# Kernel optimization log

Measured on AMD Instinct MI355X. Metric: run time of the kernel, lower is better.

Reference implementation:

```python
import jax, jax.numpy as jnp
import numpy as np

N_NODES = 50000


def gcn_layer(x, src, dst, ew, W, b, n_nodes):
    # PyG GCNConv: add self-loops (weight 1), symmetric deg^-1/2 normalization,
    # linear transform, scatter-add aggregation at destination, then bias.
    loop = jnp.arange(n_nodes, dtype=src.dtype)
    s = jnp.concatenate([src, loop])
    d = jnp.concatenate([dst, loop])
    w = jnp.concatenate([ew, jnp.ones((n_nodes,), dtype=ew.dtype)])
    deg = jax.ops.segment_sum(w, d, num_segments=n_nodes)  # [N]
    dinv = jnp.where(deg > 0, jax.lax.rsqrt(jnp.where(deg > 0, deg, 1.0)), 0.0)
    norm = dinv[s] * w * dinv[d]  # [E+N]
    h = x @ W  # [N, out]
    msg = h[s] * norm[:, None]  # gather + scale, [E+N, out]
    out = jax.ops.segment_sum(msg, d, num_segments=n_nodes)  # scatter-add
    return out + b


def setup_inputs() -> dict:
    key = jax.random.key(0)
    k1, k2, k3, k4, k5, k6, k7 = jax.random.split(key, 7)
    N, E, C_IN, C_OUT = N_NODES, 600000, 128, 128
    x = jax.random.normal(k1, (N, C_IN), dtype=jnp.float32)
    edge_index = jax.random.randint(k2, (2, E), 0, N, dtype=jnp.int64)
    edge_weight = jax.random.uniform(k3, (E,), dtype=jnp.float32)
    # Glorot-style init like PyG's Linear default
    s1 = 1.0 / np.sqrt(C_IN)
    s2 = 1.0 / np.sqrt(C_OUT)
    W1 = jax.random.uniform(k4, (C_IN, C_OUT), jnp.float32, -s1, s1)
    b1 = jnp.zeros((C_OUT,), dtype=jnp.float32)
    W2 = jax.random.uniform(k5, (C_OUT, C_OUT), jnp.float32, -s2, s2)
    b2 = jnp.zeros((C_OUT,), dtype=jnp.float32)
    return {"x": x, "edge_index": edge_index, "edge_weight": edge_weight,
            "W1": W1, "b1": b1, "W2": W2, "b2": b2}


def reference(x, edge_index, edge_weight, W1, b1, W2, b2):
    src, dst = edge_index[0], edge_index[1]
    h = jax.nn.relu(gcn_layer(x, src, dst, edge_weight, W1, b1, N_NODES))
    return jax.nn.relu(gcn_layer(h, src, dst, edge_weight, W2, b2, N_NODES))
```

## Files before the change

kernel.cpp:

```cpp
#include <hip/hip_runtime.h>
#include <math.h>

#define CH   128
#define CH4  32
#define TPB  256
#define SCANB 1024
#define WIMG 16384
#define NREP 4

typedef __attribute__((ext_vector_type(8))) short short8;
typedef __attribute__((ext_vector_type(4))) float floatx4;

static __device__ __forceinline__ unsigned short f2bf(float f) {
    unsigned u = __float_as_uint(f);
    return (unsigned short)((u + 0x7fffu + ((u >> 16) & 1u)) >> 16);
}
static __device__ __forceinline__ float bf2f(unsigned short s) {
    return __uint_as_float(((unsigned)s) << 16);
}
static __device__ __forceinline__ float4 bf4_to_f4(ushort4 u) {
    return make_float4(bf2f(u.x), bf2f(u.y), bf2f(u.z), bf2f(u.w));
}

__global__ void k_prep(const float* __restrict__ W1, const float* __restrict__ W2,
                       short* __restrict__ Wsplit) {
    int i = blockIdx.x * blockDim.x + threadIdx.x;
    if (i >= 2 * CH * CH) return;
    int layer = i >> 14;
    int idx   = i & 16383;
    int k = idx >> 7, c = idx & 127;
    float w = (layer ? W2 : W1)[k * CH + c];
    unsigned short hi = f2bf(w);
    unsigned short lo = f2bf(w - bf2f(hi));
    int colh = c >> 6, nn = c & 63;
    int kt = k >> 5, q = (k & 31) >> 3, j = k & 7;
    int ns = nn >> 4, ln = q * 16 + (nn & 15);
    size_t base = (size_t)(layer * 2 + colh) * WIMG;
    size_t off  = ((size_t)(kt * 4 + ns) * 64 + ln) * 8 + j;
    Wsplit[base + off]        = (short)hi;
    Wsplit[base + 8192 + off] = (short)lo;
}

#define STAGE_W(sW, Wfrag, tid)                                    \
    {                                                              \
        const float4* gsrc = (const float4*)(Wfrag);               \
        float4* ldst = (float4*)(sW);                              \
        _Pragma("unroll")                                          \
        for (int i = 0; i < 8; ++i)                                \
            ldst[i * TPB + (tid)] = gsrc[i * TPB + (tid)];         \
    }

static __device__ __forceinline__ void gemm_body_f32(
        const float* __restrict__ X, const short* __restrict__ Wfrag,
        unsigned short* __restrict__ H, int n, int tile, int colh, int tid) {
    __shared__ __align__(16) short sW[2][4][4][64][8];
    STAGE_W(sW, Wfrag, tid);
    __syncthreads();

    const int lane = tid & 63;
    const int wv   = tid >> 6;
    const int q    = lane >> 4;
    const int m    = lane & 15;
    const int row0 = tile * 64 + wv * 16;
    if (row0 >= n) return;

    int rrow = row0 + m;
    if (rrow > n - 1) rrow = n - 1;

    const float4* xr = (const float4*)(X + (size_t)rrow * CH);
    float4 xa[4][2];
    #pragma unroll
    for (int kt = 0; kt < 4; ++kt) {
        xa[kt][0] = xr[kt * 8 + q * 2 + 0];
        xa[kt][1] = xr[kt * 8 + q * 2 + 1];
    }

    floatx4 acc[4];
    #pragma unroll
    for (int ns = 0; ns < 4; ++ns) acc[ns] = (floatx4){0.f, 0.f, 0.f, 0.f};

    #pragma unroll
    for (int kt = 0; kt < 4; ++kt) {
        float xf[8] = { xa[kt][0].x, xa[kt][0].y, xa[kt][0].z, xa[kt][0].w,
                        xa[kt][1].x, xa[kt][1].y, xa[kt][1].z, xa[kt][1].w };
        short8 ah, al;
        #pragma unroll
        for (int j = 0; j < 8; ++j) {
            float v = xf[j];
            unsigned short h = f2bf(v);
            ah[j] = (short)h;
            al[j] = (short)f2bf(v - bf2f(h));
        }
        #pragma unroll
        for (int ns = 0; ns < 4; ++ns) {
            short8 bh = *(const short8*)&sW[0][kt][ns][lane][0];
            short8 bl = *(const short8*)&sW[1][kt][ns][lane][0];
            acc[ns] = __builtin_amdgcn_mfma_f32_16x16x32_bf16(ah, bh, acc[ns], 0, 0, 0);
            acc[ns] = __builtin_amdgcn_mfma_f32_16x16x32_bf16(al, bh, acc[ns], 0, 0, 0);
            acc[ns] = __builtin_amdgcn_mfma_f32_16x16x32_bf16(ah, bl, acc[ns], 0, 0, 0);
        }
    }

    #pragma unroll
    for (int ns = 0; ns < 4; ++ns) {
        #pragma unroll
        for (int reg = 0; reg < 4; ++reg) {
            int r = row0 + q * 4 + reg;
            if (r < n)
                H[(size_t)r * CH + colh * 64 + ns * 16 + m] = f2bf(acc[ns][reg]);
        }
    }
}

static __device__ __forceinline__ void gemm_body_bf(
        const unsigned short* __restrict__ X, const short* __restrict__ Wfrag,
        unsigned short* __restrict__ H, int n, int tile, int colh, int tid) {
    __shared__ __align__(16) short sW[2][4][4][64][8];
    STAGE_W(sW, Wfrag, tid);
    __syncthreads();

    const int lane = tid & 63;
    const int wv   = tid >> 6;
    const int q    = lane >> 4;
    const int m    = lane & 15;
    const int row0 = tile * 64 + wv * 16;
    if (row0 >= n) return;

    int rrow = row0 + m;
    if (rrow > n - 1) rrow = n - 1;

    const short8* xr8 = (const short8*)(X + (size_t)rrow * CH);
    short8 a[4];
    #pragma unroll
    for (int kt = 0; kt < 4; ++kt) a[kt] = xr8[kt * 4 + q];

    floatx4 acc[4];
    #pragma unroll
    for (int ns = 0; ns < 4; ++ns) acc[ns] = (floatx4){0.f, 0.f, 0.f, 0.f};

    #pragma unroll
    for (int kt = 0; kt < 4; ++kt) {
        #pragma unroll
        for (int ns = 0; ns < 4; ++ns) {
            short8 bh = *(const short8*)&sW[0][kt][ns][lane][0];
            short8 bl = *(const short8*)&sW[1][kt][ns][lane][0];
            acc[ns] = __builtin_amdgcn_mfma_f32_16x16x32_bf16(a[kt], bh, acc[ns], 0, 0, 0);
            acc[ns] = __builtin_amdgcn_mfma_f32_16x16x32_bf16(a[kt], bl, acc[ns], 0, 0, 0);
        }
    }

    #pragma unroll
    for (int ns = 0; ns < 4; ++ns) {
        #pragma unroll
        for (int reg = 0; reg < 4; ++reg) {
            int r = row0 + q * 4 + reg;
            if (r < n)
                H[(size_t)r * CH + colh * 64 + ns * 16 + m] = f2bf(acc[ns][reg]);
        }
    }
}

__global__ __launch_bounds__(TPB, 4)
void k_gemm_rank(const float* __restrict__ X, const short* __restrict__ Wsplit,
                 unsigned short* __restrict__ H, int n,
                 const int* __restrict__ dst, const float* __restrict__ ew,
                 int* __restrict__ counts_rep, float* __restrict__ deg_rep,
                 int* __restrict__ rank, int E, int nbE, int Np) {
    int bx = blockIdx.x;
    if (bx < nbE) {
        int e = bx * TPB + threadIdx.x;
        if (e < E) {
            int d = dst[e];
            if ((unsigned)d < (unsigned)n) {
                int rep = e & (NREP - 1);
                rank[e] = atomicAdd(&counts_rep[rep * Np + d], 1);
                unsafeAtomicAdd(&deg_rep[rep * Np + d], ew[e]);
            }
        }
    } else {
        bx -= nbE;
        int colh = bx & 1;
        gemm_body_f32(X, Wsplit + (size_t)colh * WIMG, H, n, bx >> 1, colh,
                      threadIdx.x);
    }
}

__global__ __launch_bounds__(TPB, 4)
void k_gemm_bf(const unsigned short* __restrict__ X, const short* __restrict__ Wsplit,
               unsigned short* __restrict__ H, int n) {
    int colh = (int)blockIdx.x & 1;
    gemm_body_bf(X, Wsplit + (size_t)colh * WIMG, H, n,
                 (int)blockIdx.x >> 1, colh, threadIdx.x);
}

__global__ __launch_bounds__(SCANB)
void k_scan1(const int* __restrict__ counts_rep, const float* __restrict__ deg_rep,
             int Np, int* __restrict__ counts_tot, int4* __restrict__ repoff,
             int* __restrict__ row_start, float* __restrict__ dinv,
             int* __restrict__ partials, int* __restrict__ pp_s,
             int* __restrict__ done, int nb, int n) {
    __shared__ int s[SCANB];
    __shared__ int slast;
    int gid = blockIdx.x * SCANB + threadIdx.x;
    int c0 = 0, c1 = 0, c2 = 0, c3 = 0;
    if (gid < n) {
        c0 = counts_rep[gid];
        c1 = counts_rep[Np + gid];
        c2 = counts_rep[2 * Np + gid];
        c3 = counts_rep[3 * Np + gid];
        float dsum = 1.0f + deg_rep[gid] + deg_rep[Np + gid]
                   + deg_rep[2 * Np + gid] + deg_rep[3 * Np + gid];
        dinv[gid] = rsqrtf(dsum);
    }
    int v = c0 + c1 + c2 + c3;
    s[threadIdx.x] = v;
    __syncthreads();
    for (int off = 1; off < SCANB; off <<= 1) {
        int t = (threadIdx.x >= off) ? s[threadIdx.x - off] : 0;
        __syncthreads();
        s[threadIdx.x] += t;
        __syncthreads();
    }
    if (gid < n) {
        row_start[gid]  = s[threadIdx.x] - v;
        counts_tot[gid] = v;
        repoff[gid]     = make_int4(0, c0, c0 + c1, c0 + c1 + c2);
    }
    if (threadIdx.x == SCANB - 1) {
        partials[blockIdx.x] = s[SCANB - 1];
        __threadfence();
        int old = atomicAdd(done, 1);
        slast = (old == nb - 1);
    }
    __syncthreads();
    if (slast && threadIdx.x < 64) {
        int pv = (threadIdx.x < nb) ? atomicAdd(&partials[threadIdx.x], 0) : 0;
        int inc = pv;
        #pragma unroll
        for (int off = 1; off < 64; off <<= 1) {
            int t = __shfl_up(inc, off, 64);
            if ((threadIdx.x & 63) >= off) inc += t;
        }
        if (threadIdx.x < nb) pp_s[threadIdx.x] = inc - pv;
    }
}

__global__ void k_fill(const int* __restrict__ src, const int* __restrict__ dst,
                       const float* __restrict__ ew, const int* __restrict__ row_start,
                       const int* __restrict__ pp_s, const int4* __restrict__ repoff,
                       const int* __restrict__ rank, int2* __restrict__ edges,
                       int E, int n) {
    int e = blockIdx.x * blockDim.x + threadIdx.x;
    if (e >= E) return;
    int s = src[e], d = dst[e];
    if ((unsigned)s >= (unsigned)n || (unsigned)d >= (unsigned)n) return;
    int rep = e & (NREP - 1);
    int4 ro = repoff[d];
    int roa[4] = {ro.x, ro.y, ro.z, ro.w};
    int base = row_start[d] + pp_s[d >> 10];
    edges[base + roa[rep] + rank[e]] = make_int2(s, __float_as_int(ew[e]));
}

template<int RELU_OUT, int FIXUP, int OUT_BF16>
__global__ __launch_bounds__(TPB)
void k_aggregate(const unsigned short* __restrict__ h, const int* __restrict__ row_start,
                 const int* __restrict__ pp_s, const int* __restrict__ counts,
                 int2* __restrict__ edges, const float* __restrict__ dinv,
                 const float* __restrict__ bias, void* __restrict__ out, int n) {
    int t = blockIdx.x * blockDim.x + threadIdx.x;
    int node = t >> 5;
    if (node >= n) return;
    int tx = t & 31;

    const ushort4* h4 = (const ushort4*)h;
    float di = dinv[node];
    float4 b  = ((const float4*)bias)[tx];
    float4 hv = bf4_to_f4(h4[(size_t)node * CH4 + tx]);
    float4 acc = make_float4(0.f, 0.f, 0.f, 0.f);

    int j   = row_start[node] + pp_s[node >> 10];
    int end = j + counts[node];

    for (; j + 8 <= end; j += 8) {
        int2 e[8];
        #pragma unroll
        for (int i = 0; i < 8; ++i) e[i] = edges[j + i];
        ushort4 g[8];
        #pragma unroll
        for (int i = 0; i < 8; ++i) g[i] = h4[(size_t)e[i].x * CH4 + tx];
        float w[8];
        #pragma unroll
        for (int i = 0; i < 8; ++i) {
            w[i] = __int_as_float(e[i].y);
            if (FIXUP) w[i] *= dinv[e[i].x];
        }
        if (FIXUP && tx == 0) {
            #pragma unroll
            for (int i = 0; i < 8; ++i) edges[j + i].y = __float_as_int(w[i]);
        }
        #pragma unroll
        for (int i = 0; i < 8; ++i) {
            float4 gf = bf4_to_f4(g[i]);
            acc.x += gf.x * w[i]; acc.y += gf.y * w[i];
            acc.z += gf.z * w[i]; acc.w += gf.w * w[i];
        }
    }
    if (j + 4 <= end) {
        int2 e[4];
        #pragma unroll
        for (int i = 0; i < 4; ++i) e[i] = edges[j + i];
        ushort4 g[4];
        #pragma unroll
        for (int i = 0; i < 4; ++i) g[i] = h4[(size_t)e[i].x * CH4 + tx];
        float w[4];
        #pragma unroll
        for (int i = 0; i < 4; ++i) {
            w[i] = __int_as_float(e[i].y);
            if (FIXUP) w[i] *= dinv[e[i].x];
        }
        if (FIXUP && tx == 0) {
            #pragma unroll
            for (int i = 0; i < 4; ++i) edges[j + i].y = __float_as_int(w[i]);
        }
        #pragma unroll
        for (int i = 0; i < 4; ++i) {
            float4 gf = bf4_to_f4(g[i]);
            acc.x += gf.x * w[i]; acc.y += gf.y * w[i];
            acc.z += gf.z * w[i]; acc.w += gf.w * w[i];
        }
        j += 4;
    }
    for (; j < end; ++j) {
        int2 e0 = edges[j];
        float w0 = __int_as_float(e0.y);
        if (FIXUP) w0 *= dinv[e0.x];
        if (FIXUP && tx == 0) edges[j].y = __float_as_int(w0);
        float4 gf = bf4_to_f4(h4[(size_t)e0.x * CH4 + tx]);
        acc.x += gf.x * w0; acc.y += gf.y * w0;
        acc.z += gf.z * w0; acc.w += gf.w * w0;
    }

    float sc = di * di;
    float4 o = make_float4(hv.x * sc + b.x + di * acc.x,
                           hv.y * sc + b.y + di * acc.y,
                           hv.z * sc + b.z + di * acc.z,
                           hv.w * sc + b.w + di * acc.w);
    if (RELU_OUT) {
        o.x = fmaxf(o.x, 0.f); o.y = fmaxf(o.y, 0.f);
        o.z = fmaxf(o.z, 0.f); o.w = fmaxf(o.w, 0.f);
    }
    if (OUT_BF16) {
        ushort4 u = make_ushort4(f2bf(o.x), f2bf(o.y), f2bf(o.z), f2bf(o.w));
        ((ushort4*)out)[(size_t)node * CH4 + tx] = u;
    } else {
        ((float4*)out)[(size_t)node * CH4 + tx] = o;
    }
}

extern "C" void kernel_launch(void* const* d_in, const int* in_sizes, int n_in,
                              void* d_out, int out_size, void* d_ws, size_t ws_size,
                              hipStream_t stream) {
    const float* x  = (const float*)d_in[0];
    const int*   ei = (const int*)d_in[1];
    const float* ew = (const float*)d_in[2];
    const float* W1 = (const float*)d_in[3];
    const float* b1 = (const float*)d_in[4];
    const float* W2 = (const float*)d_in[5];
    const float* b2 = (const float*)d_in[6];
    float* out = (float*)d_out;

    const int N = in_sizes[0] / CH;
    const int E = in_sizes[2];
    const int* src = ei;
    const int* dst = ei + E;

    size_t Np = ((size_t)N + 255) & ~(size_t)255;
    size_t Ep = ((size_t)E + 63) & ~(size_t)63;
    float* ws          = (float*)d_ws;
    float* dinv        = ws;
    unsigned short* h  = (unsigned short*)(dinv + Np);
    unsigned short* o1 = h + (size_t)N * CH;
    int*   counts_rep  = (int*)(o1 + (size_t)N * CH);
    float* deg_rep     = (float*)(counts_rep + NREP * Np);
    int*   done        = (int*)(deg_rep + NREP * Np);
    size_t zero_bytes  = (size_t)(2 * NREP) * Np * 4 + 256;
    int*  counts_tot   = done + 64;
    int*  row_start    = counts_tot + Np;
    int4* repoff       = (int4*)(row_start + Np);
    int*  rank         = (int*)(repoff + Np);
    int*  partials     = rank + Ep;
    int*  pp_s         = partials + 64;
    int2* edges        = (int2*)(pp_s + 64);
    short* Wsplit      = (short*)(edges + E);

    const int nbE    = (E + TPB - 1) / TPB;
    const int nbAgg  = (int)(((size_t)N * 32 + TPB - 1) / TPB);
    const int nbScan = (N + SCANB - 1) / SCANB;
    const int nbGemm2 = 2 * ((N + 63) / 64);
    const int nbPrep  = (2 * CH * CH + TPB - 1) / TPB;

    hipMemsetAsync(counts_rep, 0, zero_bytes, stream);
    k_prep     <<<nbPrep, TPB, 0, stream>>>(W1, W2, Wsplit);

    k_gemm_rank<<<nbE + nbGemm2, TPB, 0, stream>>>(x, Wsplit, h, N, dst, ew,
                                                   counts_rep, deg_rep, rank,
                                                   E, nbE, (int)Np);
    k_scan1    <<<nbScan, SCANB, 0, stream>>>(counts_rep, deg_rep, (int)Np,
                                              counts_tot, repoff, row_start,
                                              dinv, partials, pp_s, done,
                                              nbScan, N);
    k_fill     <<<nbE, TPB, 0, stream>>>(src, dst, ew, row_start, pp_s, repoff,
                                         rank, edges, E, N);

    k_aggregate<1,1,1><<<nbAgg, TPB, 0, stream>>>(h, row_start, pp_s, counts_tot,
                                                  edges, dinv, b1, o1, N);
    k_gemm_bf         <<<nbGemm2, TPB, 0, stream>>>(o1, Wsplit + 2 * WIMG, h, N);
    k_aggregate<1,0,0><<<nbAgg, TPB, 0, stream>>>(h, row_start, pp_s, counts_tot,
                                                  edges, dinv, b2, out, N);
}
```

Measured before the change: 247.6 us.

## Fuse layer-1 aggregation with layer-2 GEMM and compute degrees from CSR

Layer-1 aggregation and the layer-2 GEMM now run in one kernel. Each block aggregates 64 nodes into shared memory as bf16 and multiplies them by W2 with MFMA, so the intermediate o1 buffer never goes to global memory. The float atomic degree accumulation is removed: a new k_deg kernel sums edge weights from the CSR edges after fill. The atomic count replicas rise from 4 to 8 to spread contention. The tradeoffs are lower occupancy from the larger shared footprint, an extra kernel launch, and one thread per node serially scanning its edge list for the degree.

```diff
diff --git a/kernel.cpp b/kernel.cpp
--- a/kernel.cpp
+++ b/kernel.cpp
@@ -6,7 +6,7 @@
 #define TPB  256
 #define SCANB 1024
 #define WIMG 16384
-#define NREP 4
+#define NREP 8
 
 typedef __attribute__((ext_vector_type(8))) short short8;
 typedef __attribute__((ext_vector_type(4))) float floatx4;
@@ -112,59 +112,10 @@
     }
 }
 
-static __device__ __forceinline__ void gemm_body_bf(
-        const unsigned short* __restrict__ X, const short* __restrict__ Wfrag,
-        unsigned short* __restrict__ H, int n, int tile, int colh, int tid) {
-    __shared__ __align__(16) short sW[2][4][4][64][8];
-    STAGE_W(sW, Wfrag, tid);
-    __syncthreads();
-
-    const int lane = tid & 63;
-    const int wv   = tid >> 6;
-    const int q    = lane >> 4;
-    const int m    = lane & 15;
-    const int row0 = tile * 64 + wv * 16;
-    if (row0 >= n) return;
-
-    int rrow = row0 + m;
-    if (rrow > n - 1) rrow = n - 1;
-
-    const short8* xr8 = (const short8*)(X + (size_t)rrow * CH);
-    short8 a[4];
-    #pragma unroll
-    for (int kt = 0; kt < 4; ++kt) a[kt] = xr8[kt * 4 + q];
-
-    floatx4 acc[4];
-    #pragma unroll
-    for (int ns = 0; ns < 4; ++ns) acc[ns] = (floatx4){0.f, 0.f, 0.f, 0.f};
-
-    #pragma unroll
-    for (int kt = 0; kt < 4; ++kt) {
-        #pragma unroll
-        for (int ns = 0; ns < 4; ++ns) {
-            short8 bh = *(const short8*)&sW[0][kt][ns][lane][0];
-            short8 bl = *(const short8*)&sW[1][kt][ns][lane][0];
-            acc[ns] = __builtin_amdgcn_mfma_f32_16x16x32_bf16(a[kt], bh, acc[ns], 0, 0, 0);
-            acc[ns] = __builtin_amdgcn_mfma_f32_16x16x32_bf16(a[kt], bl, acc[ns], 0, 0, 0);
-        }
-    }
-
-    #pragma unroll
-    for (int ns = 0; ns < 4; ++ns) {
-        #pragma unroll
-        for (int reg = 0; reg < 4; ++reg) {
-            int r = row0 + q * 4 + reg;
-            if (r < n)
-                H[(size_t)r * CH + colh * 64 + ns * 16 + m] = f2bf(acc[ns][reg]);
-        }
-    }
-}
-
 __global__ __launch_bounds__(TPB, 4)
 void k_gemm_rank(const float* __restrict__ X, const short* __restrict__ Wsplit,
                  unsigned short* __restrict__ H, int n,
-                 const int* __restrict__ dst, const float* __restrict__ ew,
-                 int* __restrict__ counts_rep, float* __restrict__ deg_rep,
+                 const int* __restrict__ dst, int* __restrict__ counts_rep,
                  int* __restrict__ rank, int E, int nbE, int Np) {
     int bx = blockIdx.x;
     if (bx < nbE) {
@@ -174,7 +125,6 @@
             if ((unsigned)d < (unsigned)n) {
                 int rep = e & (NREP - 1);
                 rank[e] = atomicAdd(&counts_rep[rep * Np + d], 1);
-                unsafeAtomicAdd(&deg_rep[rep * Np + d], ew[e]);
             }
         }
     } else {
@@ -185,34 +135,21 @@
     }
 }
 
-__global__ __launch_bounds__(TPB, 4)
-void k_gemm_bf(const unsigned short* __restrict__ X, const short* __restrict__ Wsplit,
-               unsigned short* __restrict__ H, int n) {
-    int colh = (int)blockIdx.x & 1;
-    gemm_body_bf(X, Wsplit + (size_t)colh * WIMG, H, n,
-                 (int)blockIdx.x >> 1, colh, threadIdx.x);
-}
-
 __global__ __launch_bounds__(SCANB)
-void k_scan1(const int* __restrict__ counts_rep, const float* __restrict__ deg_rep,
-             int Np, int* __restrict__ counts_tot, int4* __restrict__ repoff,
-             int* __restrict__ row_start, float* __restrict__ dinv,
-             int* __restrict__ partials, int* __restrict__ pp_s,
-             int* __restrict__ done, int nb, int n) {
+void k_scan1(const int* __restrict__ counts_rep, int Np,
+             int* __restrict__ counts_tot, int* __restrict__ repoff8,
+             int* __restrict__ row_start, int* __restrict__ partials,
+             int* __restrict__ pp_s, int* __restrict__ done, int nb, int n) {
     __shared__ int s[SCANB];
     __shared__ int slast;
     int gid = blockIdx.x * SCANB + threadIdx.x;
-    int c0 = 0, c1 = 0, c2 = 0, c3 = 0;
-    if (gid < n) {
-        c0 = counts_rep[gid];
-        c1 = counts_rep[Np + gid];
-        c2 = counts_rep[2 * Np + gid];
-        c3 = counts_rep[3 * Np + gid];
-        float dsum = 1.0f + deg_rep[gid] + deg_rep[Np + gid]
-                   + deg_rep[2 * Np + gid] + deg_rep[3 * Np + gid];
-        dinv[gid] = rsqrtf(dsum);
-    }
-    int v = c0 + c1 + c2 + c3;
+    int c[NREP];
+    int v = 0;
+    #pragma unroll
+    for (int r = 0; r < NREP; ++r) {
+        c[r] = (gid < n) ? counts_rep[r * Np + gid] : 0;
+        v += c[r];
+    }
     s[threadIdx.x] = v;
     __syncthreads();
     for (int off = 1; off < SCANB; off <<= 1) {
@@ -224,7 +161,12 @@
     if (gid < n) {
         row_start[gid]  = s[threadIdx.x] - v;
         counts_tot[gid] = v;
-        repoff[gid]     = make_int4(0, c0, c0 + c1, c0 + c1 + c2);
+        int pre = 0;
+        int ro[NREP];
+        #pragma unroll
+        for (int r = 0; r < NREP; ++r) { ro[r] = pre; pre += c[r]; }
+        ((int4*)repoff8)[gid * 2 + 0] = make_int4(ro[0], ro[1], ro[2], ro[3]);
+        ((int4*)repoff8)[gid * 2 + 1] = make_int4(ro[4], ro[5], ro[6], ro[7]);
     }
     if (threadIdx.x == SCANB - 1) {
         partials[blockIdx.x] = s[SCANB - 1];
@@ -247,7 +189,7 @@
 
 __global__ void k_fill(const int* __restrict__ src, const int* __restrict__ dst,
                        const float* __restrict__ ew, const int* __restrict__ row_start,
-                       const int* __restrict__ pp_s, const int4* __restrict__ repoff,
+                       const int* __restrict__ pp_s, const int* __restrict__ repoff8,
                        const int* __restrict__ rank, int2* __restrict__ edges,
                        int E, int n) {
     int e = blockIdx.x * blockDim.x + threadIdx.x;
@@ -255,29 +197,30 @@
     int s = src[e], d = dst[e];
     if ((unsigned)s >= (unsigned)n || (unsigned)d >= (unsigned)n) return;
     int rep = e & (NREP - 1);
-    int4 ro = repoff[d];
-    int roa[4] = {ro.x, ro.y, ro.z, ro.w};
-    int base = row_start[d] + pp_s[d >> 10];
-    edges[base + roa[rep] + rank[e]] = make_int2(s, __float_as_int(ew[e]));
-}
-
-template<int RELU_OUT, int FIXUP, int OUT_BF16>
-__global__ __launch_bounds__(TPB)
-void k_aggregate(const unsigned short* __restrict__ h, const int* __restrict__ row_start,
-                 const int* __restrict__ pp_s, const int* __restrict__ counts,
-                 int2* __restrict__ edges, const float* __restrict__ dinv,
-                 const float* __restrict__ bias, void* __restrict__ out, int n) {
-    int t = blockIdx.x * blockDim.x + threadIdx.x;
-    int node = t >> 5;
-    if (node >= n) return;
-    int tx = t & 31;
-
-    const ushort4* h4 = (const ushort4*)h;
+    int base = row_start[d] + pp_s[d >> 10] + repoff8[d * NREP + rep];
+    edges[base + rank[e]] = make_int2(s, __float_as_int(ew[e]));
+}
+
+__global__ void k_deg(const int* __restrict__ row_start, const int* __restrict__ pp_s,
+                      const int* __restrict__ counts, const int2* __restrict__ edges,
+                      float* __restrict__ dinv, int n) {
+    int i = blockIdx.x * blockDim.x + threadIdx.x;
+    if (i >= n) return;
+    int j = row_start[i] + pp_s[i >> 10], end = j + counts[i];
+    float sum = 1.0f;
+    for (; j < end; ++j) sum += __int_as_float(edges[j].y);
+    dinv[i] = rsqrtf(sum);
+}
+
+template<int FIXUP>
+static __device__ __forceinline__ float4 agg_node(
+        const ushort4* __restrict__ h4, int2* __restrict__ edges,
+        const float* __restrict__ dinv, const float4 b, int node, int tx,
+        const int* __restrict__ row_start, const int* __restrict__ pp_s,
+        const int* __restrict__ counts) {
     float di = dinv[node];
-    float4 b  = ((const float4*)bias)[tx];
     float4 hv = bf4_to_f4(h4[(size_t)node * CH4 + tx]);
     float4 acc = make_float4(0.f, 0.f, 0.f, 0.f);
-
     int j   = row_start[node] + pp_s[node >> 10];
     int end = j + counts[node];
 
@@ -341,20 +284,105 @@
     }
 
     float sc = di * di;
-    float4 o = make_float4(hv.x * sc + b.x + di * acc.x,
-                           hv.y * sc + b.y + di * acc.y,
-                           hv.z * sc + b.z + di * acc.z,
-                           hv.w * sc + b.w + di * acc.w);
-    if (RELU_OUT) {
-        o.x = fmaxf(o.x, 0.f); o.y = fmaxf(o.y, 0.f);
-        o.z = fmaxf(o.z, 0.f); o.w = fmaxf(o.w, 0.f);
-    }
-    if (OUT_BF16) {
-        ushort4 u = make_ushort4(f2bf(o.x), f2bf(o.y), f2bf(o.z), f2bf(o.w));
-        ((ushort4*)out)[(size_t)node * CH4 + tx] = u;
-    } else {
-        ((float4*)out)[(size_t)node * CH4 + tx] = o;
-    }
+    return make_float4(hv.x * sc + b.x + di * acc.x,
+                       hv.y * sc + b.y + di * acc.y,
+                       hv.z * sc + b.z + di * acc.z,
+                       hv.w * sc + b.w + di * acc.w);
+}
+
+__global__ __launch_bounds__(TPB, 3)
+void k_agg_gemm(const unsigned short* __restrict__ h,
+                const int* __restrict__ row_start, const int* __restrict__ pp_s,
+                const int* __restrict__ counts, int2* __restrict__ edges,
+                const float* __restrict__ dinv, const float* __restrict__ bias,
+                const short* __restrict__ W2frag,
+                unsigned short* __restrict__ Hout, int n) {
+    __shared__ __align__(16) short sW[2][4][4][64][8];
+    __shared__ __align__(16) unsigned short sA[64][136];
+    const int tid = threadIdx.x;
+
+    {
+        const float4* g0 = (const float4*)(W2frag);
+        const float4* g1 = (const float4*)(W2frag + WIMG);
+        float4* d0 = (float4*)&sW[0][0][0][0][0];
+        float4* d1 = (float4*)&sW[1][0][0][0][0];
+        #pragma unroll
+        for (int i = 0; i < 4; ++i) {
+            d0[i * TPB + tid] = g0[i * TPB + tid];
+            d1[i * TPB + tid] = g1[i * TPB + tid];
+        }
+    }
+
+    const int lane = tid & 63;
+    const int wv   = tid >> 6;
+    const int half = lane >> 5;
+    const int tx   = lane & 31;
+    const ushort4* h4 = (const ushort4*)h;
+    const float4 b = ((const float4*)bias)[tx];
+
+    for (int nd = 0; nd < 8; ++nd) {
+        int nl   = wv * 16 + nd * 2 + half;
+        int node = blockIdx.x * 64 + nl;
+        ushort4 u = make_ushort4(0, 0, 0, 0);
+        if (node < n) {
+            float4 o = agg_node<1>(h4, edges, dinv, b, node, tx,
+                                   row_start, pp_s, counts);
+            u = make_ushort4(f2bf(fmaxf(o.x, 0.f)), f2bf(fmaxf(o.y, 0.f)),
+                             f2bf(fmaxf(o.z, 0.f)), f2bf(fmaxf(o.w, 0.f)));
+        }
+        *(ushort4*)&sA[nl][tx * 4] = u;
+    }
+    __syncthreads();
+
+    const int q = lane >> 4;
+    const int m = lane & 15;
+    short8 a[4];
+    #pragma unroll
+    for (int kt = 0; kt < 4; ++kt)
+        a[kt] = *(const short8*)&sA[wv * 16 + m][kt * 32 + q * 8];
+
+    floatx4 acc[8];
+    #pragma unroll
+    for (int s2 = 0; s2 < 8; ++s2) acc[s2] = (floatx4){0.f, 0.f, 0.f, 0.f};
+
+    #pragma unroll
+    for (int kt = 0; kt < 4; ++kt) {
+        #pragma unroll
+        for (int s2 = 0; s2 < 8; ++s2) {
+            short8 bh = *(const short8*)&sW[s2 >> 2][kt][s2 & 3][lane][0];
+            acc[s2] = __builtin_amdgcn_mfma_f32_16x16x32_bf16(a[kt], bh, acc[s2], 0, 0, 0);
+        }
+    }
+
+    const int row0 = blockIdx.x * 64 + wv * 16;
+    #pragma unroll
+    for (int s2 = 0; s2 < 8; ++s2) {
+        int col = (s2 >> 2) * 64 + (s2 & 3) * 16 + m;
+        #pragma unroll
+        for (int reg = 0; reg < 4; ++reg) {
+            int r = row0 + q * 4 + reg;
+            if (r < n)
+                Hout[(size_t)r * CH + col] = f2bf(acc[s2][reg]);
+        }
+    }
+}
+
+__global__ __launch_bounds__(TPB)
+void k_aggregate2(const unsigned short* __restrict__ h,
+                  const int* __restrict__ row_start, const int* __restrict__ pp_s,
+                  const int* __restrict__ counts, int2* __restrict__ edges,
+                  const float* __restrict__ dinv, const float* __restrict__ bias,
+                  float* __restrict__ out, int n) {
+    int t = blockIdx.x * blockDim.x + threadIdx.x;
+    int node = t >> 5;
+    if (node >= n) return;
+    int tx = t & 31;
+    const float4 b = ((const float4*)bias)[tx];
+    float4 o = agg_node<0>((const ushort4*)h, edges, dinv, b, node, tx,
+                           row_start, pp_s, counts);
+    o.x = fmaxf(o.x, 0.f); o.y = fmaxf(o.y, 0.f);
+    o.z = fmaxf(o.z, 0.f); o.w = fmaxf(o.w, 0.f);
+    ((float4*)out)[(size_t)node * CH4 + tx] = o;
 }
 
 extern "C" void kernel_launch(void* const* d_in, const int* in_sizes, int n_in,
@@ -379,42 +407,43 @@
     float* ws          = (float*)d_ws;
     float* dinv        = ws;
     unsigned short* h  = (unsigned short*)(dinv + Np);
-    unsigned short* o1 = h + (size_t)N * CH;
-    int*   counts_rep  = (int*)(o1 + (size_t)N * CH);
-    float* deg_rep     = (float*)(counts_rep + NREP * Np);
-    int*   done        = (int*)(deg_rep + NREP * Np);
-    size_t zero_bytes  = (size_t)(2 * NREP) * Np * 4 + 256;
+    unsigned short* h2 = h + (size_t)N * CH;
+    int*   counts_rep  = (int*)(h2 + (size_t)N * CH);
+    int*   done        = counts_rep + NREP * Np;
+    size_t zero_bytes  = (size_t)NREP * Np * 4 + 256;
     int*  counts_tot   = done + 64;
     int*  row_start    = counts_tot + Np;
-    int4* repoff       = (int4*)(row_start + Np);
-    int*  rank         = (int*)(repoff + Np);
+    int*  repoff8      = row_start + Np;
+    int*  rank         = repoff8 + NREP * Np;
     int*  partials     = rank + Ep;
     int*  pp_s         = partials + 64;
     int2* edges        = (int2*)(pp_s + 64);
     short* Wsplit      = (short*)(edges + E);
 
+    const int nbN    = (N + TPB - 1) / TPB;
     const int nbE    = (E + TPB - 1) / TPB;
     const int nbAgg  = (int)(((size_t)N * 32 + TPB - 1) / TPB);
     const int nbScan = (N + SCANB - 1) / SCANB;
-    const int nbGemm2 = 2 * ((N + 63) / 64);
+    const int nbT64  = (N + 63) / 64;
+    const int nbGemm2 = 2 * nbT64;
     const int nbPrep  = (2 * CH * CH + TPB - 1) / TPB;
 
     hipMemsetAsync(counts_rep, 0, zero_bytes, stream);
     k_prep     <<<nbPrep, TPB, 0, stream>>>(W1, W2, Wsplit);
 
-    k_gemm_rank<<<nbE + nbGemm2, TPB, 0, stream>>>(x, Wsplit, h, N, dst, ew,
-                                                   counts_rep, deg_rep, rank,
-                                                   E, nbE, (int)Np);
-    k_scan1    <<<nbScan, SCANB, 0, stream>>>(counts_rep, deg_rep, (int)Np,
-                                              counts_tot, repoff, row_start,
-                                              dinv, partials, pp_s, done,
-                                              nbScan, N);
-    k_fill     <<<nbE, TPB, 0, stream>>>(src, dst, ew, row_start, pp_s, repoff,
+    k_gemm_rank<<<nbE + nbGemm2, TPB, 0, stream>>>(x, Wsplit, h, N, dst,
+                                                   counts_rep, rank, E, nbE, (int)Np);
+    k_scan1    <<<nbScan, SCANB, 0, stream>>>(counts_rep, (int)Np, counts_tot,
+                                              repoff8, row_start, partials,
+                                              pp_s, done, nbScan, N);
+    k_fill     <<<nbE, TPB, 0, stream>>>(src, dst, ew, row_start, pp_s, repoff8,
                                          rank, edges, E, N);
-
-    k_aggregate<1,1,1><<<nbAgg, TPB, 0, stream>>>(h, row_start, pp_s, counts_tot,
-                                                  edges, dinv, b1, o1, N);
-    k_gemm_bf         <<<nbGemm2, TPB, 0, stream>>>(o1, Wsplit + 2 * WIMG, h, N);
-    k_aggregate<1,0,0><<<nbAgg, TPB, 0, stream>>>(h, row_start, pp_s, counts_tot,
-                                                  edges, dinv, b2, out, N);
-}
+    k_deg      <<<nbN, TPB, 0, stream>>>(row_start, pp_s, counts_tot, edges,
+                                         dinv, N);
+
+    k_agg_gemm <<<nbT64, TPB, 0, stream>>>(h, row_start, pp_s, counts_tot,
+                                           edges, dinv, b1,
+                                           Wsplit + 2 * (size_t)WIMG, h2, N);
+    k_aggregate2<<<nbAgg, TPB, 0, stream>>>(h2, row_start, pp_s, counts_tot,
+                                            edges, dinv, b2, out, N);
+}
```

New measurement: 251.4 us. About the same (+1.5%).
